# Performance work log

Measured on AMD Instinct MI355X. Metric: run time of the kernel, lower is better.

## Reference

```python
import jax, jax.numpy as jnp
import numpy as np

N = 50000      # num nodes
E = 800000     # num edges (before self loops)
B = 50         # num graphs in batch
F_IN = 15
C = 64         # hidden_channels
H = 4          # num_heads
NEG_SLOPE = 0.2  # PyG GATConv default


def setup_inputs() -> dict:
    key = jax.random.key(0)
    ks = jax.random.split(key, 32)
    s = 0.05
    inp = {
        "x": jax.random.normal(ks[0], (N, F_IN), dtype=jnp.float32),
        "edge_index": jax.random.randint(ks[1], (2, E), 0, N, dtype=jnp.int32),
        "batch": jnp.sort(jax.random.randint(ks[2], (N,), 0, B, dtype=jnp.int32)),
        "W1": jax.random.normal(ks[3], (F_IN, H * C)) * s,
        "aS1": jax.random.normal(ks[4], (H, C)) * s,
        "aD1": jax.random.normal(ks[5], (H, C)) * s,
        "b1": jnp.zeros((H * C,)),
        "W2": jax.random.normal(ks[6], (H * C, H * C)) * s,
        "aS2": jax.random.normal(ks[7], (H, C)) * s,
        "aD2": jax.random.normal(ks[8], (H, C)) * s,
        "b2": jnp.zeros((H * C,)),
        # GAT layer 3: 256 -> 64, 1 head
        "W3": jax.random.normal(ks[9], (H * C, C)) * s,
        "aS3": jax.random.normal(ks[10], (1, C)) * s,
        "aD3": jax.random.normal(ks[11], (1, C)) * s,
        "b3": jnp.zeros((C,)),
        # node attention MLP: 64 -> 32 -> 1
        "Wna1": jax.random.normal(ks[12], (C, 32)) * s,
        "bna1": jnp.zeros((32,)),
        "Wna2": jax.random.normal(ks[13], (32, 1)) * s,
        "bna2": jnp.zeros((1,)),
        # graph classifier: 128 -> 128 -> 64 -> 1
        "Wc1": jax.random.normal(ks[14], (2 * C, 128)) * s,
        "bc1": jnp.zeros((128,)),
        "Wc2": jax.random.normal(ks[15], (128, 64)) * s,
        "bc2": jnp.zeros((64,)),
        "Wc3": jax.random.normal(ks[16], (64, 1)) * s,
        "bc3": jnp.zeros((1,)),
    }
    return inp


def _gat_conv(x, src, dst, W, a_src, a_dst, b, heads, ch):
    """PyG-style GATConv (add_self_loops=True, negative_slope=0.2, eval mode)."""
    n = x.shape[0]
    h = (x @ W).reshape(n, heads, ch)               # [N, H, C]
    alpha_s = jnp.einsum('nhc,hc->nh', h, a_src)    # per-node src score
    alpha_d = jnp.einsum('nhc,hc->nh', h, a_dst)
    loops = jnp.arange(n, dtype=src.dtype)
    s = jnp.concatenate([src, loops])               # [E+N]
    d = jnp.concatenate([dst, loops])
    e = jax.nn.leaky_relu(alpha_s[s] + alpha_d[d], NEG_SLOPE)   # [E+N, H]
    # segment softmax over incoming edges of each dst node
    m = jax.ops.segment_max(e, d, num_segments=n)
    ex = jnp.exp(e - m[d])
    denom = jax.ops.segment_sum(ex, d, num_segments=n)
    alpha = ex / denom[d]                           # [E+N, H]
    msg = h[s] * alpha[:, :, None]                  # [E+N, H, C]
    out = jax.ops.segment_sum(msg, d, num_segments=n)  # [N, H, C]
    return out.reshape(n, heads * ch) + b


def reference(x, edge_index, batch, W1, aS1, aD1, b1, W2, aS2, aD2, b2,
              W3, aS3, aD3, b3, Wna1, bna1, Wna2, bna2,
              Wc1, bc1, Wc2, bc2, Wc3, bc3):
    src, dst = edge_index[0], edge_index[1]
    x1 = jax.nn.elu(_gat_conv(x, src, dst, W1, aS1, aD1, b1, H, C))
    x2 = jax.nn.elu(_gat_conv(x1, src, dst, W2, aS2, aD2, b2, H, C))
    x3 = jax.nn.elu(_gat_conv(x2, src, dst, W3, aS3, aD3, b3, 1, C))  # [N, 64]

    # node attention: MLP then softmax over ALL nodes (dim=0, as in source)
    na = jax.nn.relu(x3 @ Wna1 + bna1) @ Wna2 + bna2   # [N, 1]
    node_attention = jax.nn.softmax(na, axis=0)

    # graph pooling
    ones = jnp.ones((x3.shape[0],), dtype=x3.dtype)
    cnt = jax.ops.segment_sum(ones, batch, num_segments=B)         # [B]
    mean = jax.ops.segment_sum(x3, batch, num_segments=B) / jnp.maximum(cnt, 1.0)[:, None]
    mx = jax.ops.segment_max(x3, batch, num_segments=B)
    mx = jnp.where(cnt[:, None] > 0, mx, 0.0)
    g = jnp.concatenate([mean, mx], axis=1)                        # [B, 128]

    h1 = jax.nn.relu(g @ Wc1 + bc1)
    h2 = jax.nn.relu(h1 @ Wc2 + bc2)
    risk = jax.nn.sigmoid(h2 @ Wc3 + bc3)                          # [B, 1]
    return (risk, node_attention)
```

## Files before the change

### kernel.cpp

```cpp
#include <hip/hip_runtime.h>
#include <math.h>

#define NN 50000
#define EE 800000
#define ETOT (EE + NN)
#define BB 50
#define PC 16

typedef unsigned short u16;
typedef __attribute__((ext_vector_type(8))) short short8;
typedef __attribute__((ext_vector_type(4))) float floatx4;

__device__ __forceinline__ float b2f(u16 u) {
  return __int_as_float(((int)u) << 16);
}
__device__ __forceinline__ u16 f2b(float f) {
  unsigned u = __float_as_uint(f);
  unsigned r = (u + 0x7fffu + ((u >> 16) & 1u)) >> 16;
  return (u16)r;
}
__device__ __forceinline__ float readlane_f(float v, int l) {
  return __int_as_float(__builtin_amdgcn_readlane(__float_as_int(v), l));
}
__device__ __forceinline__ float blo(unsigned w) { return __uint_as_float(w << 16); }
__device__ __forceinline__ float bhi(unsigned w) { return __uint_as_float(w & 0xffff0000u); }

__global__ void count_kernel(const int* __restrict__ ei, int* __restrict__ cnt) {
  int e = blockIdx.x * blockDim.x + threadIdx.x;
  if (e >= ETOT) return;
  int d = (e < EE) ? ei[EE + e] : (e - EE);
  atomicAdd(&cnt[d], 1);
}

__global__ void scan1_kernel(const int* __restrict__ cnt, int* __restrict__ rowp,
                             int* __restrict__ part) {
  __shared__ int s[512];
  int t = threadIdx.x;
  int i = blockIdx.x * 512 + t;
  int v = (i < NN) ? cnt[i] : 0;
  s[t] = v;
  __syncthreads();
  for (int off = 1; off < 512; off <<= 1) {
    int add = (t >= off) ? s[t - off] : 0;
    __syncthreads();
    s[t] += add;
    __syncthreads();
  }
  if (i < NN) rowp[i] = s[t] - v;
  if (t == 511) part[blockIdx.x] = s[511];
}

__global__ void scan2_kernel(int* part, int* rowp) {
  int run = 0;
  for (int b = 0; b < 98; ++b) { int v = part[b]; part[b] = run; run += v; }
  rowp[NN] = run;
}

__global__ void scan3_kernel(int* __restrict__ rowp, const int* __restrict__ part) {
  int i = blockIdx.x * 512 + threadIdx.x;
  if (i < NN) rowp[i] += part[blockIdx.x];
}

__global__ void fill_kernel(const int* __restrict__ ei, const int* __restrict__ rowp,
                            int* __restrict__ cur, int* __restrict__ col) {
  int e = blockIdx.x * blockDim.x + threadIdx.x;
  if (e >= ETOT) return;
  int s, d;
  if (e < EE) { s = ei[e]; d = ei[EE + e]; } else { s = e - EE; d = s; }
  int p = atomicAdd(&cur[d], 1);
  col[rowp[d] + p] = s;
}

__global__ void prep_kernel(const float* __restrict__ x, const float* __restrict__ W1,
                            const float* __restrict__ W2, const float* __restrict__ W3,
                            u16* __restrict__ xb, u16* __restrict__ W1t,
                            u16* __restrict__ W2t, u16* __restrict__ W3t) {
  const int T0 = NN * 32, T1 = T0 + 8192, T2 = T1 + 65536, T3 = T2 + 16384;
  int i = blockIdx.x * 256 + threadIdx.x;
  if (i < T0) {
    int n = i >> 5, c = i & 31;
    xb[i] = (c < 15) ? f2b(x[n * 15 + c]) : (u16)0;
  } else if (i < T1) {
    int j = i - T0, n = j >> 5, k = j & 31;
    W1t[j] = (k < 15) ? f2b(W1[k * 256 + n]) : (u16)0;
  } else if (i < T2) {
    int j = i - T1, n = j >> 8, k = j & 255;
    W2t[j] = f2b(W2[k * 256 + n]);
  } else if (i < T3) {
    int j = i - T2, n = j >> 8, k = j & 255;
    W3t[j] = f2b(W3[k * 64 + n]);
  }
}

__global__ __launch_bounds__(256) void gemm_bf16_kernel(
    const u16* __restrict__ A, const u16* __restrict__ Bt, u16* __restrict__ C,
    int M, int K, int N) {
  __shared__ u16 Al[128][40];
  __shared__ u16 Bl[64][40];
  int R0 = blockIdx.x * 128, C0 = blockIdx.y * 64;
  int wid = threadIdx.x >> 6, lane = threadIdx.x & 63;
  int wr = (wid >> 1) * 64, wc = (wid & 1) * 32;
  int lrow = lane & 15, lk8 = (lane >> 4) * 8;
  floatx4 acc[4][2];
#pragma unroll
  for (int i = 0; i < 4; ++i)
#pragma unroll
    for (int j = 0; j < 2; ++j) acc[i][j] = (floatx4){0.f, 0.f, 0.f, 0.f};

  for (int k0 = 0; k0 < K; k0 += 32) {
#pragma unroll
    for (int c = threadIdx.x; c < 1024; c += 256) {
      int r = c >> 3, off = (c & 7) * 4;
      int gr = R0 + r;
      ushort4 va = make_ushort4(0, 0, 0, 0);
      if (gr < M) va = *(const ushort4*)&A[(size_t)gr * K + k0 + off];
      *(ushort4*)&Al[r][off] = va;
      if (c < 512)
        *(ushort4*)&Bl[r][off] = *(const ushort4*)&Bt[(size_t)(C0 + r) * K + k0 + off];
    }
    __syncthreads();
    short8 a[4], b[2];
#pragma unroll
    for (int i = 0; i < 4; ++i) a[i] = *(const short8*)&Al[wr + i * 16 + lrow][lk8];
#pragma unroll
    for (int j = 0; j < 2; ++j) b[j] = *(const short8*)&Bl[wc + j * 16 + lrow][lk8];
#pragma unroll
    for (int i = 0; i < 4; ++i)
#pragma unroll
      for (int j = 0; j < 2; ++j)
        acc[i][j] = __builtin_amdgcn_mfma_f32_16x16x32_bf16(a[i], b[j], acc[i][j], 0, 0, 0);
    __syncthreads();
  }
  int rq = (lane >> 4) * 4;
#pragma unroll
  for (int i = 0; i < 4; ++i)
#pragma unroll
    for (int j = 0; j < 2; ++j)
#pragma unroll
      for (int q = 0; q < 4; ++q) {
        int gr = R0 + wr + i * 16 + rq + q;
        if (gr < M) C[(size_t)gr * N + C0 + wc + j * 16 + lrow] = f2b(acc[i][j][q]);
      }
}

template <int H>
__global__ void score_kernel(const u16* __restrict__ h, const float* __restrict__ aS,
                             const float* __restrict__ aD, float* __restrict__ as_o,
                             float* __restrict__ ad_o) {
  const int CT = H * 64;
  int wid = threadIdx.x >> 6, lane = threadIdx.x & 63;
  int n = blockIdx.x * (blockDim.x >> 6) + wid;
  if (n >= NN) return;
  float ps[H], pd[H];
#pragma unroll
  for (int j = 0; j < H; ++j) {
    float hv = b2f(h[(size_t)n * CT + lane + 64 * j]);
    ps[j] = hv * aS[lane + 64 * j];
    pd[j] = hv * aD[lane + 64 * j];
  }
#pragma unroll
  for (int j = 0; j < H; ++j) {
    for (int o = 32; o; o >>= 1) {
      ps[j] += __shfl_xor(ps[j], o, 64);
      pd[j] += __shfl_xor(pd[j], o, 64);
    }
  }
  if (lane == 0) {
#pragma unroll
    for (int j = 0; j < H; ++j) {
      as_o[(size_t)n * H + j] = ps[j];
      ad_o[(size_t)n * H + j] = pd[j];
    }
  }
}

__global__ __launch_bounds__(256) void agg4_kernel(
    const u16* __restrict__ h, const float* __restrict__ as_i,
    const float* __restrict__ ad_i, const int* __restrict__ rowp,
    const int* __restrict__ col, const float* __restrict__ bias,
    u16* __restrict__ xo) {
  __shared__ float exs[4][64][4];
  int wid = threadIdx.x >> 6, lane = threadIdx.x & 63;
  int d = blockIdx.x * 4 + wid;
  int rp0 = rowp[d], deg = rowp[d + 1] - rp0;
  float4 add = *(const float4*)&ad_i[(size_t)d * 4];
  int hj = lane >> 4;
  int lq = lane << 2;
  float acc0 = 0.f, acc1 = 0.f, acc2 = 0.f, acc3 = 0.f;
  float den0 = 0.f, den1 = 0.f, den2 = 0.f, den3 = 0.f;

  for (int base = 0; base < deg; base += 64) {
    int i = base + lane;
    bool valid = i < deg;
    int s = valid ? col[rp0 + i] : 0;
    float4 asv = *(const float4*)&as_i[(size_t)s * 4];
    float e0 = asv.x + add.x, e1 = asv.y + add.y, e2 = asv.z + add.z, e3 = asv.w + add.w;
    e0 = (e0 > 0.f) ? e0 : 0.2f * e0;
    e1 = (e1 > 0.f) ? e1 : 0.2f * e1;
    e2 = (e2 > 0.f) ? e2 : 0.2f * e2;
    e3 = (e3 > 0.f) ? e3 : 0.2f * e3;
    float x0 = valid ? __expf(e0) : 0.f;
    float x1 = valid ? __expf(e1) : 0.f;
    float x2 = valid ? __expf(e2) : 0.f;
    float x3 = valid ? __expf(e3) : 0.f;
    den0 += x0; den1 += x1; den2 += x2; den3 += x3;
    *(float4*)&exs[wid][lane][0] = make_float4(x0, x1, x2, x3);
    __threadfence_block();
    int cnt = min(64, deg - base);
    int k4 = cnt & ~3;
    for (int k = 0; k < k4; k += 4) {
      int s0 = __builtin_amdgcn_readlane(s, k);
      int s1 = __builtin_amdgcn_readlane(s, k + 1);
      int s2 = __builtin_amdgcn_readlane(s, k + 2);
      int s3 = __builtin_amdgcn_readlane(s, k + 3);
      float q0 = exs[wid][k][hj];
      float q1 = exs[wid][k + 1][hj];
      float q2 = exs[wid][k + 2][hj];
      float q3 = exs[wid][k + 3][hj];
      uint2 w0 = *(const uint2*)&h[(size_t)s0 * 256 + lq];
      uint2 w1 = *(const uint2*)&h[(size_t)s1 * 256 + lq];
      uint2 w2 = *(const uint2*)&h[(size_t)s2 * 256 + lq];
      uint2 w3 = *(const uint2*)&h[(size_t)s3 * 256 + lq];
      acc0 += q0 * blo(w0.x); acc1 += q0 * bhi(w0.x);
      acc2 += q0 * blo(w0.y); acc3 += q0 * bhi(w0.y);
      acc0 += q1 * blo(w1.x); acc1 += q1 * bhi(w1.x);
      acc2 += q1 * blo(w1.y); acc3 += q1 * bhi(w1.y);
      acc0 += q2 * blo(w2.x); acc1 += q2 * bhi(w2.x);
      acc2 += q2 * blo(w2.y); acc3 += q2 * bhi(w2.y);
      acc0 += q3 * blo(w3.x); acc1 += q3 * bhi(w3.x);
      acc2 += q3 * blo(w3.y); acc3 += q3 * bhi(w3.y);
    }
    for (int k = k4; k < cnt; ++k) {
      int sk = __builtin_amdgcn_readlane(s, k);
      float qk = exs[wid][k][hj];
      uint2 wk = *(const uint2*)&h[(size_t)sk * 256 + lq];
      acc0 += qk * blo(wk.x); acc1 += qk * bhi(wk.x);
      acc2 += qk * blo(wk.y); acc3 += qk * bhi(wk.y);
    }
  }
#pragma unroll
  for (int o = 32; o; o >>= 1) {
    den0 += __shfl_xor(den0, o, 64);
    den1 += __shfl_xor(den1, o, 64);
    den2 += __shfl_xor(den2, o, 64);
    den3 += __shfl_xor(den3, o, 64);
  }
  float den = (hj == 0) ? den0 : (hj == 1) ? den1 : (hj == 2) ? den2 : den3;
  float inv = 1.f / den;
  float4 bv = *(const float4*)&bias[lq];
  float v0 = acc0 * inv + bv.x;
  float v1 = acc1 * inv + bv.y;
  float v2 = acc2 * inv + bv.z;
  float v3 = acc3 * inv + bv.w;
  v0 = (v0 > 0.f) ? v0 : expm1f(v0);
  v1 = (v1 > 0.f) ? v1 : expm1f(v1);
  v2 = (v2 > 0.f) ? v2 : expm1f(v2);
  v3 = (v3 > 0.f) ? v3 : expm1f(v3);
  ushort4 o4;
  o4.x = f2b(v0); o4.y = f2b(v1); o4.z = f2b(v2); o4.w = f2b(v3);
  ((ushort4*)xo)[(size_t)d * 64 + lane] = o4;
}

__global__ __launch_bounds__(256) void agg1_kernel(
    const u16* __restrict__ h, const float* __restrict__ as_i,
    const float* __restrict__ ad_i, const int* __restrict__ rowp,
    const int* __restrict__ col, const float* __restrict__ bias,
    float* __restrict__ xo) {
  int wid = threadIdx.x >> 6, lane = threadIdx.x & 63;
  int d = blockIdx.x * 4 + wid;
  int rp0 = rowp[d], deg = rowp[d + 1] - rp0;
  float add = ad_i[d];
  float acc = 0.f, den = 0.f;
  for (int base = 0; base < deg; base += 64) {
    int i = base + lane;
    bool valid = i < deg;
    int s = valid ? col[rp0 + i] : 0;
    float e = as_i[s] + add;
    e = (e > 0.f) ? e : 0.2f * e;
    float ex = valid ? __expf(e) : 0.f;
    den += ex;
    int cnt = min(64, deg - base);
    int k4 = cnt & ~3;
    for (int k = 0; k < k4; k += 4) {
      int s0 = __builtin_amdgcn_readlane(s, k);
      int s1 = __builtin_amdgcn_readlane(s, k + 1);
      int s2 = __builtin_amdgcn_readlane(s, k + 2);
      int s3 = __builtin_amdgcn_readlane(s, k + 3);
      float q0 = readlane_f(ex, k);
      float q1 = readlane_f(ex, k + 1);
      float q2 = readlane_f(ex, k + 2);
      float q3 = readlane_f(ex, k + 3);
      float h0 = b2f(h[(size_t)s0 * 64 + lane]);
      float h1 = b2f(h[(size_t)s1 * 64 + lane]);
      float h2 = b2f(h[(size_t)s2 * 64 + lane]);
      float h3 = b2f(h[(size_t)s3 * 64 + lane]);
      acc += q0 * h0 + q1 * h1 + q2 * h2 + q3 * h3;
    }
    for (int k = k4; k < cnt; ++k) {
      int sk = __builtin_amdgcn_readlane(s, k);
      float qk = readlane_f(ex, k);
      acc += qk * b2f(h[(size_t)sk * 64 + lane]);
    }
  }
#pragma unroll
  for (int o = 32; o; o >>= 1) den += __shfl_xor(den, o, 64);
  float v = acc / den + bias[lane];
  v = (v > 0.f) ? v : expm1f(v);
  xo[(size_t)d * 64 + lane] = v;
}

__global__ void na_kernel(const float* __restrict__ x3, const float* __restrict__ W1,
                          const float* __restrict__ b1, const float* __restrict__ W2,
                          const float* __restrict__ b2, float* __restrict__ na,
                          float* __restrict__ gsum) {
  __shared__ float Ws[64 * 32];
  __shared__ float W2s[32];
  __shared__ float sred[4];
  for (int i = threadIdx.x; i < 2048; i += blockDim.x) Ws[i] = W1[i];
  if (threadIdx.x < 32) W2s[threadIdx.x] = W2[threadIdx.x];
  __syncthreads();
  int n = blockIdx.x * blockDim.x + threadIdx.x;
  float ez = 0.f;
  if (n < NN) {
    float hid[32];
#pragma unroll
    for (int j = 0; j < 32; ++j) hid[j] = b1[j];
    for (int k = 0; k < 64; ++k) {
      float xv = x3[(size_t)n * 64 + k];
#pragma unroll
      for (int j = 0; j < 32; ++j) hid[j] += xv * Ws[k * 32 + j];
    }
    float z = b2[0];
#pragma unroll
    for (int j = 0; j < 32; ++j) z += fmaxf(hid[j], 0.f) * W2s[j];
    ez = __expf(z);
    na[n] = ez;
  }
  float acc = ez;
  for (int o = 32; o; o >>= 1) acc += __shfl_xor(acc, o, 64);
  int wid = threadIdx.x >> 6, lane = threadIdx.x & 63;
  if (lane == 0) sred[wid] = acc;
  __syncthreads();
  if (threadIdx.x == 0) atomicAdd(gsum, sred[0] + sred[1] + sred[2] + sred[3]);
}

__global__ void na_write_kernel(const float* __restrict__ na, const float* __restrict__ gsum,
                                float* __restrict__ out) {
  int n = blockIdx.x * blockDim.x + threadIdx.x;
  if (n >= NN) return;
  out[n] = na[n] / gsum[0];
}

__global__ void pool1_kernel(const float* __restrict__ x3, const int* __restrict__ batch,
                             float* __restrict__ ppsum, float* __restrict__ ppmax) {
  int b = blockIdx.x, c = blockIdx.y;
  int lane = threadIdx.x & 63, wid = threadIdx.x >> 6;
  int lo = 0, hi = NN;
  while (lo < hi) { int m = (lo + hi) >> 1; if (batch[m] < b) lo = m + 1; else hi = m; }
  int start = lo;
  lo = start; hi = NN;
  while (lo < hi) { int m = (lo + hi) >> 1; if (batch[m] < b + 1) lo = m + 1; else hi = m; }
  int end = lo;
  int len = end - start;
  int c0 = start + (int)((long)len * c / PC);
  int c1 = start + (int)((long)len * (c + 1) / PC);
  float acc = 0.f, mx = -INFINITY;
  for (int n = c0 + wid; n < c1; n += 4) {
    float v = x3[(size_t)n * 64 + lane];
    acc += v;
    mx = fmaxf(mx, v);
  }
  __shared__ float ssum[4][64], smax[4][64];
  ssum[wid][lane] = acc;
  smax[wid][lane] = mx;
  __syncthreads();
  if (wid == 0) {
    acc = ssum[0][lane] + ssum[1][lane] + ssum[2][lane] + ssum[3][lane];
    mx = fmaxf(fmaxf(smax[0][lane], smax[1][lane]), fmaxf(smax[2][lane], smax[3][lane]));
    size_t o = ((size_t)c * BB + b) * 64 + lane;
    ppsum[o] = acc;
    ppmax[o] = mx;
  }
}

__global__ void pool2_kernel(const float* __restrict__ ppsum, const float* __restrict__ ppmax,
                             const int* __restrict__ batch, float* __restrict__ psum,
                             float* __restrict__ pmax, float* __restrict__ pcnt) {
  int b = blockIdx.x, lane = threadIdx.x;
  float s = 0.f, m = -INFINITY;
#pragma unroll
  for (int c = 0; c < PC; ++c) {
    size_t o = ((size_t)c * BB + b) * 64 + lane;
    s += ppsum[o];
    m = fmaxf(m, ppmax[o]);
  }
  psum[b * 64 + lane] = s;
  pmax[b * 64 + lane] = m;
  if (lane == 0) {
    int lo = 0, hi = NN;
    while (lo < hi) { int mid = (lo + hi) >> 1; if (batch[mid] < b) lo = mid + 1; else hi = mid; }
    int start = lo;
    lo = start; hi = NN;
    while (lo < hi) { int mid = (lo + hi) >> 1; if (batch[mid] < b + 1) lo = mid + 1; else hi = mid; }
    pcnt[b] = (float)(lo - start);
  }
}

__global__ void cls_kernel(const float* __restrict__ psum, const float* __restrict__ pmax,
                           const float* __restrict__ pcnt, const float* __restrict__ Wc1,
                           const float* __restrict__ bc1, const float* __restrict__ Wc2,
                           const float* __restrict__ bc2, const float* __restrict__ Wc3,
                           const float* __restrict__ bc3, float* __restrict__ out) {
  __shared__ float g[128], h1[128], h2[64];
  int b = blockIdx.x, t = threadIdx.x;
  float cnt = pcnt[b];
  if (t < 64) {
    g[t] = (cnt > 0.f) ? psum[b * 64 + t] / fmaxf(cnt, 1.f) : 0.f;
    g[64 + t] = (cnt > 0.f) ? pmax[b * 64 + t] : 0.f;
  }
  __syncthreads();
  float v = bc1[t];
  for (int k = 0; k < 128; ++k) v += g[k] * Wc1[k * 128 + t];
  h1[t] = fmaxf(v, 0.f);
  __syncthreads();
  if (t < 64) {
    float v2 = bc2[t];
    for (int k = 0; k < 128; ++k) v2 += h1[k] * Wc2[k * 64 + t];
    h2[t] = fmaxf(v2, 0.f);
  }
  __syncthreads();
  if (t == 0) {
    float z = bc3[0];
    for (int k = 0; k < 64; ++k) z += h2[k] * Wc3[k];
    out[b] = 1.f / (1.f + expf(-z));
  }
}

extern "C" void kernel_launch(void* const* d_in, const int* in_sizes, int n_in,
                              void* d_out, int out_size, void* d_ws, size_t ws_size,
                              hipStream_t stream) {
  const float* x    = (const float*)d_in[0];
  const int*   ei   = (const int*)d_in[1];
  const int*   batch= (const int*)d_in[2];
  const float* W1 = (const float*)d_in[3];
  const float* aS1= (const float*)d_in[4];
  const float* aD1= (const float*)d_in[5];
  const float* b1 = (const float*)d_in[6];
  const float* W2 = (const float*)d_in[7];
  const float* aS2= (const float*)d_in[8];
  const float* aD2= (const float*)d_in[9];
  const float* b2 = (const float*)d_in[10];
  const float* W3 = (const float*)d_in[11];
  const float* aS3= (const float*)d_in[12];
  const float* aD3= (const float*)d_in[13];
  const float* b3 = (const float*)d_in[14];
  const float* Wna1=(const float*)d_in[15];
  const float* bna1=(const float*)d_in[16];
  const float* Wna2=(const float*)d_in[17];
  const float* bna2=(const float*)d_in[18];
  const float* Wc1=(const float*)d_in[19];
  const float* bc1=(const float*)d_in[20];
  const float* Wc2=(const float*)d_in[21];
  const float* bc2=(const float*)d_in[22];
  const float* Wc3=(const float*)d_in[23];
  const float* bc3=(const float*)d_in[24];
  float* out = (float*)d_out;

  char* w = (char*)d_ws;
  size_t off = 0;
  auto alloc = [&](size_t bytes) {
    void* p = w + off;
    off = (off + bytes + 255) & ~(size_t)255;
    return p;
  };
  u16* xb   = (u16*)alloc((size_t)NN * 32 * 2);
  u16* bufA = (u16*)alloc((size_t)NN * 256 * 2);
  u16* bufB = (u16*)alloc((size_t)NN * 256 * 2);
  u16* W1t  = (u16*)alloc((size_t)256 * 32 * 2);
  u16* W2t  = (u16*)alloc((size_t)256 * 256 * 2);
  u16* W3t  = (u16*)alloc((size_t)64 * 256 * 2);
  float* asb  = (float*)alloc((size_t)NN * 4 * 4);
  float* adb  = (float*)alloc((size_t)NN * 4 * 4);
  float* nab  = (float*)alloc((size_t)NN * 4);
  int* rowp = (int*)alloc((size_t)(NN + 1) * 4);
  int* cntb = (int*)alloc((size_t)NN * 4);
  int* curb = (int*)alloc((size_t)NN * 4);
  float* gsum = (float*)alloc(256);
  size_t zspan = (size_t)((char*)gsum + 256 - (char*)cntb);
  int* colb = (int*)alloc((size_t)ETOT * 4);
  int* part = (int*)alloc(98 * 4);
  float* psum = (float*)alloc((size_t)BB * 64 * 4);
  float* pmax = (float*)alloc((size_t)BB * 64 * 4);
  float* pcnt = (float*)alloc((size_t)BB * 4);
  float* ppsum = (float*)alloc((size_t)PC * BB * 64 * 4);
  float* ppmax = (float*)alloc((size_t)PC * BB * 64 * 4);
  float* x3 = (float*)bufB;
  (void)ws_size; (void)in_sizes; (void)n_in; (void)out_size;

  hipMemsetAsync(cntb, 0, zspan, stream);

  count_kernel<<<(ETOT + 255) / 256, 256, 0, stream>>>(ei, cntb);
  scan1_kernel<<<98, 512, 0, stream>>>(cntb, rowp, part);
  scan2_kernel<<<1, 1, 0, stream>>>(part, rowp);
  scan3_kernel<<<98, 512, 0, stream>>>(rowp, part);
  fill_kernel<<<(ETOT + 255) / 256, 256, 0, stream>>>(ei, rowp, curb, colb);

  const int PREP_TOT = NN * 32 + 8192 + 65536 + 16384;
  prep_kernel<<<(PREP_TOT + 255) / 256, 256, 0, stream>>>(x, W1, W2, W3, xb, W1t, W2t, W3t);

  const int GX = (NN + 127) / 128;
  gemm_bf16_kernel<<<dim3(GX, 4), 256, 0, stream>>>(xb, W1t, bufA, NN, 32, 256);
  score_kernel<4><<<12500, 256, 0, stream>>>(bufA, aS1, aD1, asb, adb);
  agg4_kernel<<<12500, 256, 0, stream>>>(bufA, asb, adb, rowp, colb, b1, bufB);
  gemm_bf16_kernel<<<dim3(GX, 4), 256, 0, stream>>>(bufB, W2t, bufA, NN, 256, 256);
  score_kernel<4><<<12500, 256, 0, stream>>>(bufA, aS2, aD2, asb, adb);
  agg4_kernel<<<12500, 256, 0, stream>>>(bufA, asb, adb, rowp, colb, b2, bufB);
  gemm_bf16_kernel<<<dim3(GX, 1), 256, 0, stream>>>(bufB, W3t, bufA, NN, 256, 64);
  score_kernel<1><<<12500, 256, 0, stream>>>(bufA, aS3, aD3, asb, adb);
  agg1_kernel<<<12500, 256, 0, stream>>>(bufA, asb, adb, rowp, colb, b3, x3);

  na_kernel<<<(NN + 255) / 256, 256, 0, stream>>>(x3, Wna1, bna1, Wna2, bna2, nab, gsum);
  na_write_kernel<<<(NN + 255) / 256, 256, 0, stream>>>(nab, gsum, out + BB);

  pool1_kernel<<<dim3(BB, PC), 256, 0, stream>>>(x3, batch, ppsum, ppmax);
  pool2_kernel<<<BB, 64, 0, stream>>>(ppsum, ppmax, batch, psum, pmax, pcnt);
  cls_kernel<<<BB, 128, 0, stream>>>(psum, pmax, pcnt, Wc1, bc1, Wc2, bc2, Wc3, bc3, out);
}
```

Baseline: 437.2 us.

## Fuse attention scores into GEMM epilogue, merge scans and pooling kernels

Computes per-node source/destination attention scores inside the bf16 GEMM epilogue using cross-lane shuffles, removing the three separate score kernels and their re-read of h. Rows are padded to a multiple of 128 so bounds checks in the GEMM go away, and K is tiled by 64 for the deeper layers. The three-kernel prefix scan becomes one single-block scan, pool2 and the classifier are merged, the agg1 gather loop is unrolled to 8, and the node-attention MLP loads x3 as float4. Costs are extra shared memory and shuffles in the GEMM, plus a single-block scan that runs serially over 49 elements per thread.

```diff
diff --git a/kernel.cpp b/kernel.cpp
--- a/kernel.cpp
+++ b/kernel.cpp
@@ -2,6 +2,7 @@
 #include <math.h>
 
 #define NN 50000
+#define NP 50176
 #define EE 800000
 #define ETOT (EE + NN)
 #define BB 50
@@ -32,33 +33,30 @@
   atomicAdd(&cnt[d], 1);
 }
 
-__global__ void scan1_kernel(const int* __restrict__ cnt, int* __restrict__ rowp,
-                             int* __restrict__ part) {
-  __shared__ int s[512];
+__global__ __launch_bounds__(1024) void scan_kernel(const int* __restrict__ cnt,
+                                                    int* __restrict__ rowp) {
+  __shared__ int part[1024];
   int t = threadIdx.x;
-  int i = blockIdx.x * 512 + t;
-  int v = (i < NN) ? cnt[i] : 0;
-  s[t] = v;
-  __syncthreads();
-  for (int off = 1; off < 512; off <<= 1) {
-    int add = (t >= off) ? s[t - off] : 0;
+  int base = t * 49;
+  int sum = 0;
+  for (int i = 0; i < 49; ++i) {
+    int idx = base + i;
+    if (idx < NN) sum += cnt[idx];
+  }
+  part[t] = sum;
+  __syncthreads();
+  for (int off = 1; off < 1024; off <<= 1) {
+    int add = (t >= off) ? part[t - off] : 0;
     __syncthreads();
-    s[t] += add;
+    part[t] += add;
     __syncthreads();
   }
-  if (i < NN) rowp[i] = s[t] - v;
-  if (t == 511) part[blockIdx.x] = s[511];
-}
-
-__global__ void scan2_kernel(int* part, int* rowp) {
-  int run = 0;
-  for (int b = 0; b < 98; ++b) { int v = part[b]; part[b] = run; run += v; }
-  rowp[NN] = run;
-}
-
-__global__ void scan3_kernel(int* __restrict__ rowp, const int* __restrict__ part) {
-  int i = blockIdx.x * 512 + threadIdx.x;
-  if (i < NN) rowp[i] += part[blockIdx.x];
+  int run = (t > 0) ? part[t - 1] : 0;
+  for (int i = 0; i < 49; ++i) {
+    int idx = base + i;
+    if (idx < NN) { rowp[idx] = run; run += cnt[idx]; }
+  }
+  if (t == 1023) rowp[NN] = part[1023];
 }
 
 __global__ void fill_kernel(const int* __restrict__ ei, const int* __restrict__ rowp,
@@ -75,11 +73,11 @@
                             const float* __restrict__ W2, const float* __restrict__ W3,
                             u16* __restrict__ xb, u16* __restrict__ W1t,
                             u16* __restrict__ W2t, u16* __restrict__ W3t) {
-  const int T0 = NN * 32, T1 = T0 + 8192, T2 = T1 + 65536, T3 = T2 + 16384;
+  const int T0 = NP * 32, T1 = T0 + 8192, T2 = T1 + 65536, T3 = T2 + 16384;
   int i = blockIdx.x * 256 + threadIdx.x;
   if (i < T0) {
     int n = i >> 5, c = i & 31;
-    xb[i] = (c < 15) ? f2b(x[n * 15 + c]) : (u16)0;
+    xb[i] = (n < NN && c < 15) ? f2b(x[n * 15 + c]) : (u16)0;
   } else if (i < T1) {
     int j = i - T0, n = j >> 5, k = j & 31;
     W1t[j] = (k < 15) ? f2b(W1[k * 256 + n]) : (u16)0;
@@ -92,46 +90,54 @@
   }
 }
 
+template <int BK>
 __global__ __launch_bounds__(256) void gemm_bf16_kernel(
     const u16* __restrict__ A, const u16* __restrict__ Bt, u16* __restrict__ C,
-    int M, int K, int N) {
-  __shared__ u16 Al[128][40];
-  __shared__ u16 Bl[64][40];
+    int K, int N, const float* __restrict__ aS, const float* __restrict__ aD,
+    float* __restrict__ as_o, float* __restrict__ ad_o, int Hh) {
+  __shared__ u16 Al[128][BK + 8];
+  __shared__ u16 Bl[64][BK + 8];
+  __shared__ float sS[4][64], sD[4][64];
   int R0 = blockIdx.x * 128, C0 = blockIdx.y * 64;
   int wid = threadIdx.x >> 6, lane = threadIdx.x & 63;
   int wr = (wid >> 1) * 64, wc = (wid & 1) * 32;
   int lrow = lane & 15, lk8 = (lane >> 4) * 8;
+  int rq = (lane >> 4) * 4;
+  const int Q4 = BK / 4;
+  const int nA = 128 * Q4, nB = 64 * Q4;
   floatx4 acc[4][2];
 #pragma unroll
   for (int i = 0; i < 4; ++i)
 #pragma unroll
     for (int j = 0; j < 2; ++j) acc[i][j] = (floatx4){0.f, 0.f, 0.f, 0.f};
 
-  for (int k0 = 0; k0 < K; k0 += 32) {
-#pragma unroll
-    for (int c = threadIdx.x; c < 1024; c += 256) {
-      int r = c >> 3, off = (c & 7) * 4;
-      int gr = R0 + r;
-      ushort4 va = make_ushort4(0, 0, 0, 0);
-      if (gr < M) va = *(const ushort4*)&A[(size_t)gr * K + k0 + off];
-      *(ushort4*)&Al[r][off] = va;
-      if (c < 512)
-        *(ushort4*)&Bl[r][off] = *(const ushort4*)&Bt[(size_t)(C0 + r) * K + k0 + off];
+  for (int k0 = 0; k0 < K; k0 += BK) {
+    for (int c = threadIdx.x; c < nA + nB; c += 256) {
+      if (c < nA) {
+        int r = c / Q4, o = (c % Q4) * 4;
+        *(ushort4*)&Al[r][o] = *(const ushort4*)&A[(size_t)(R0 + r) * K + k0 + o];
+      } else {
+        int c2 = c - nA;
+        int r = c2 / Q4, o = (c2 % Q4) * 4;
+        *(ushort4*)&Bl[r][o] = *(const ushort4*)&Bt[(size_t)(C0 + r) * K + k0 + o];
+      }
     }
     __syncthreads();
-    short8 a[4], b[2];
-#pragma unroll
-    for (int i = 0; i < 4; ++i) a[i] = *(const short8*)&Al[wr + i * 16 + lrow][lk8];
-#pragma unroll
-    for (int j = 0; j < 2; ++j) b[j] = *(const short8*)&Bl[wc + j * 16 + lrow][lk8];
-#pragma unroll
-    for (int i = 0; i < 4; ++i)
-#pragma unroll
-      for (int j = 0; j < 2; ++j)
-        acc[i][j] = __builtin_amdgcn_mfma_f32_16x16x32_bf16(a[i], b[j], acc[i][j], 0, 0, 0);
+#pragma unroll
+    for (int ks = 0; ks < BK / 32; ++ks) {
+      short8 a[4], b[2];
+#pragma unroll
+      for (int i = 0; i < 4; ++i) a[i] = *(const short8*)&Al[wr + i * 16 + lrow][ks * 32 + lk8];
+#pragma unroll
+      for (int j = 0; j < 2; ++j) b[j] = *(const short8*)&Bl[wc + j * 16 + lrow][ks * 32 + lk8];
+#pragma unroll
+      for (int i = 0; i < 4; ++i)
+#pragma unroll
+        for (int j = 0; j < 2; ++j)
+          acc[i][j] = __builtin_amdgcn_mfma_f32_16x16x32_bf16(a[i], b[j], acc[i][j], 0, 0, 0);
+    }
     __syncthreads();
   }
-  int rq = (lane >> 4) * 4;
 #pragma unroll
   for (int i = 0; i < 4; ++i)
 #pragma unroll
@@ -139,38 +145,34 @@
 #pragma unroll
       for (int q = 0; q < 4; ++q) {
         int gr = R0 + wr + i * 16 + rq + q;
-        if (gr < M) C[(size_t)gr * N + C0 + wc + j * 16 + lrow] = f2b(acc[i][j][q]);
+        C[(size_t)gr * N + C0 + wc + j * 16 + lrow] = f2b(acc[i][j][q]);
       }
-}
-
-template <int H>
-__global__ void score_kernel(const u16* __restrict__ h, const float* __restrict__ aS,
-                             const float* __restrict__ aD, float* __restrict__ as_o,
-                             float* __restrict__ ad_o) {
-  const int CT = H * 64;
-  int wid = threadIdx.x >> 6, lane = threadIdx.x & 63;
-  int n = blockIdx.x * (blockDim.x >> 6) + wid;
-  if (n >= NN) return;
-  float ps[H], pd[H];
-#pragma unroll
-  for (int j = 0; j < H; ++j) {
-    float hv = b2f(h[(size_t)n * CT + lane + 64 * j]);
-    ps[j] = hv * aS[lane + 64 * j];
-    pd[j] = hv * aD[lane + 64 * j];
-  }
-#pragma unroll
-  for (int j = 0; j < H; ++j) {
-    for (int o = 32; o; o >>= 1) {
-      ps[j] += __shfl_xor(ps[j], o, 64);
-      pd[j] += __shfl_xor(pd[j], o, 64);
-    }
-  }
-  if (lane == 0) {
-#pragma unroll
-    for (int j = 0; j < H; ++j) {
-      as_o[(size_t)n * H + j] = ps[j];
-      ad_o[(size_t)n * H + j] = pd[j];
-    }
+  int hb = blockIdx.y * 64;
+  float wS0 = aS[hb + wc + lrow], wS1 = aS[hb + wc + 16 + lrow];
+  float wD0 = aD[hb + wc + lrow], wD1 = aD[hb + wc + 16 + lrow];
+#pragma unroll
+  for (int i = 0; i < 4; ++i)
+#pragma unroll
+    for (int q = 0; q < 4; ++q) {
+      float vS = acc[i][0][q] * wS0 + acc[i][1][q] * wS1;
+      float vD = acc[i][0][q] * wD0 + acc[i][1][q] * wD1;
+#pragma unroll
+      for (int o = 8; o; o >>= 1) {
+        vS += __shfl_xor(vS, o, 64);
+        vD += __shfl_xor(vD, o, 64);
+      }
+      if (lrow == 0) {
+        int rl = i * 16 + rq + q;
+        sS[wid][rl] = vS;
+        sD[wid][rl] = vD;
+      }
+    }
+  __syncthreads();
+  if (threadIdx.x < 128) {
+    int p = threadIdx.x >> 6, r = threadIdx.x & 63;
+    int gr = R0 + p * 64 + r;
+    as_o[(size_t)gr * Hh + blockIdx.y] = sS[2 * p][r] + sS[2 * p + 1][r];
+    ad_o[(size_t)gr * Hh + blockIdx.y] = sD[2 * p][r] + sD[2 * p + 1][r];
   }
 }
 
@@ -280,23 +282,24 @@
     float ex = valid ? __expf(e) : 0.f;
     den += ex;
     int cnt = min(64, deg - base);
-    int k4 = cnt & ~3;
-    for (int k = 0; k < k4; k += 4) {
-      int s0 = __builtin_amdgcn_readlane(s, k);
-      int s1 = __builtin_amdgcn_readlane(s, k + 1);
-      int s2 = __builtin_amdgcn_readlane(s, k + 2);
-      int s3 = __builtin_amdgcn_readlane(s, k + 3);
-      float q0 = readlane_f(ex, k);
-      float q1 = readlane_f(ex, k + 1);
-      float q2 = readlane_f(ex, k + 2);
-      float q3 = readlane_f(ex, k + 3);
-      float h0 = b2f(h[(size_t)s0 * 64 + lane]);
-      float h1 = b2f(h[(size_t)s1 * 64 + lane]);
-      float h2 = b2f(h[(size_t)s2 * 64 + lane]);
-      float h3 = b2f(h[(size_t)s3 * 64 + lane]);
-      acc += q0 * h0 + q1 * h1 + q2 * h2 + q3 * h3;
-    }
-    for (int k = k4; k < cnt; ++k) {
+    int k8 = cnt & ~7;
+    for (int k = 0; k < k8; k += 8) {
+      int sA[8];
+      float qA[8], hv[8];
+#pragma unroll
+      for (int u = 0; u < 8; ++u) {
+        sA[u] = __builtin_amdgcn_readlane(s, k + u);
+        qA[u] = readlane_f(ex, k + u);
+      }
+#pragma unroll
+      for (int u = 0; u < 8; ++u) hv[u] = b2f(h[(size_t)sA[u] * 64 + lane]);
+      float p0 = qA[0] * hv[0] + qA[1] * hv[1];
+      float p1 = qA[2] * hv[2] + qA[3] * hv[3];
+      float p2 = qA[4] * hv[4] + qA[5] * hv[5];
+      float p3 = qA[6] * hv[6] + qA[7] * hv[7];
+      acc += (p0 + p1) + (p2 + p3);
+    }
+    for (int k = k8; k < cnt; ++k) {
       int sk = __builtin_amdgcn_readlane(s, k);
       float qk = readlane_f(ex, k);
       acc += qk * b2f(h[(size_t)sk * 64 + lane]);
@@ -325,10 +328,16 @@
     float hid[32];
 #pragma unroll
     for (int j = 0; j < 32; ++j) hid[j] = b1[j];
-    for (int k = 0; k < 64; ++k) {
-      float xv = x3[(size_t)n * 64 + k];
-#pragma unroll
-      for (int j = 0; j < 32; ++j) hid[j] += xv * Ws[k * 32 + j];
+    const float4* x4 = (const float4*)&x3[(size_t)n * 64];
+    for (int kk = 0; kk < 16; ++kk) {
+      float4 xv = x4[kk];
+#pragma unroll
+      for (int j = 0; j < 32; ++j) {
+        hid[j] += xv.x * Ws[(kk * 4 + 0) * 32 + j];
+        hid[j] += xv.y * Ws[(kk * 4 + 1) * 32 + j];
+        hid[j] += xv.z * Ws[(kk * 4 + 2) * 32 + j];
+        hid[j] += xv.w * Ws[(kk * 4 + 3) * 32 + j];
+      }
     }
     float z = b2[0];
 #pragma unroll
@@ -383,40 +392,35 @@
   }
 }
 
-__global__ void pool2_kernel(const float* __restrict__ ppsum, const float* __restrict__ ppmax,
-                             const int* __restrict__ batch, float* __restrict__ psum,
-                             float* __restrict__ pmax, float* __restrict__ pcnt) {
-  int b = blockIdx.x, lane = threadIdx.x;
-  float s = 0.f, m = -INFINITY;
-#pragma unroll
-  for (int c = 0; c < PC; ++c) {
-    size_t o = ((size_t)c * BB + b) * 64 + lane;
-    s += ppsum[o];
-    m = fmaxf(m, ppmax[o]);
-  }
-  psum[b * 64 + lane] = s;
-  pmax[b * 64 + lane] = m;
-  if (lane == 0) {
+__global__ void pool2cls_kernel(const float* __restrict__ ppsum, const float* __restrict__ ppmax,
+                                const int* __restrict__ batch, const float* __restrict__ Wc1,
+                                const float* __restrict__ bc1, const float* __restrict__ Wc2,
+                                const float* __restrict__ bc2, const float* __restrict__ Wc3,
+                                const float* __restrict__ bc3, float* __restrict__ out) {
+  __shared__ float g[128], h1[128], h2[64], scnt;
+  int b = blockIdx.x, t = threadIdx.x;
+  if (t == 0) {
     int lo = 0, hi = NN;
-    while (lo < hi) { int mid = (lo + hi) >> 1; if (batch[mid] < b) lo = mid + 1; else hi = mid; }
+    while (lo < hi) { int m = (lo + hi) >> 1; if (batch[m] < b) lo = m + 1; else hi = m; }
     int start = lo;
     lo = start; hi = NN;
-    while (lo < hi) { int mid = (lo + hi) >> 1; if (batch[mid] < b + 1) lo = mid + 1; else hi = mid; }
-    pcnt[b] = (float)(lo - start);
-  }
-}
-
-__global__ void cls_kernel(const float* __restrict__ psum, const float* __restrict__ pmax,
-                           const float* __restrict__ pcnt, const float* __restrict__ Wc1,
-                           const float* __restrict__ bc1, const float* __restrict__ Wc2,
-                           const float* __restrict__ bc2, const float* __restrict__ Wc3,
-                           const float* __restrict__ bc3, float* __restrict__ out) {
-  __shared__ float g[128], h1[128], h2[64];
-  int b = blockIdx.x, t = threadIdx.x;
-  float cnt = pcnt[b];
+    while (lo < hi) { int m = (lo + hi) >> 1; if (batch[m] < b + 1) lo = m + 1; else hi = m; }
+    scnt = (float)(lo - start);
+  }
+  float s = 0.f, m = -INFINITY;
   if (t < 64) {
-    g[t] = (cnt > 0.f) ? psum[b * 64 + t] / fmaxf(cnt, 1.f) : 0.f;
-    g[64 + t] = (cnt > 0.f) ? pmax[b * 64 + t] : 0.f;
+#pragma unroll
+    for (int c = 0; c < PC; ++c) {
+      size_t o = ((size_t)c * BB + b) * 64 + t;
+      s += ppsum[o];
+      m = fmaxf(m, ppmax[o]);
+    }
+  }
+  __syncthreads();
+  float cnt = scnt;
+  if (t < 64) {
+    g[t] = (cnt > 0.f) ? s / fmaxf(cnt, 1.f) : 0.f;
+    g[64 + t] = (cnt > 0.f) ? m : 0.f;
   }
   __syncthreads();
   float v = bc1[t];
@@ -473,14 +477,14 @@
     off = (off + bytes + 255) & ~(size_t)255;
     return p;
   };
-  u16* xb   = (u16*)alloc((size_t)NN * 32 * 2);
-  u16* bufA = (u16*)alloc((size_t)NN * 256 * 2);
-  u16* bufB = (u16*)alloc((size_t)NN * 256 * 2);
+  u16* xb   = (u16*)alloc((size_t)NP * 32 * 2);
+  u16* bufA = (u16*)alloc((size_t)NP * 256 * 2);
+  u16* bufB = (u16*)alloc((size_t)NP * 256 * 2);
   u16* W1t  = (u16*)alloc((size_t)256 * 32 * 2);
   u16* W2t  = (u16*)alloc((size_t)256 * 256 * 2);
   u16* W3t  = (u16*)alloc((size_t)64 * 256 * 2);
-  float* asb  = (float*)alloc((size_t)NN * 4 * 4);
-  float* adb  = (float*)alloc((size_t)NN * 4 * 4);
+  float* asb  = (float*)alloc((size_t)NP * 4 * 4);
+  float* adb  = (float*)alloc((size_t)NP * 4 * 4);
   float* nab  = (float*)alloc((size_t)NN * 4);
   int* rowp = (int*)alloc((size_t)(NN + 1) * 4);
   int* cntb = (int*)alloc((size_t)NN * 4);
@@ -488,10 +492,6 @@
   float* gsum = (float*)alloc(256);
   size_t zspan = (size_t)((char*)gsum + 256 - (char*)cntb);
   int* colb = (int*)alloc((size_t)ETOT * 4);
-  int* part = (int*)alloc(98 * 4);
-  float* psum = (float*)alloc((size_t)BB * 64 * 4);
-  float* pmax = (float*)alloc((size_t)BB * 64 * 4);
-  float* pcnt = (float*)alloc((size_t)BB * 4);
   float* ppsum = (float*)alloc((size_t)PC * BB * 64 * 4);
   float* ppmax = (float*)alloc((size_t)PC * BB * 64 * 4);
   float* x3 = (float*)bufB;
@@ -500,29 +500,27 @@
   hipMemsetAsync(cntb, 0, zspan, stream);
 
   count_kernel<<<(ETOT + 255) / 256, 256, 0, stream>>>(ei, cntb);
-  scan1_kernel<<<98, 512, 0, stream>>>(cntb, rowp, part);
-  scan2_kernel<<<1, 1, 0, stream>>>(part, rowp);
-  scan3_kernel<<<98, 512, 0, stream>>>(rowp, part);
+  scan_kernel<<<1, 1024, 0, stream>>>(cntb, rowp);
   fill_kernel<<<(ETOT + 255) / 256, 256, 0, stream>>>(ei, rowp, curb, colb);
 
-  const int PREP_TOT = NN * 32 + 8192 + 65536 + 16384;
+  const int PREP_TOT = NP * 32 + 8192 + 65536 + 16384;
   prep_kernel<<<(PREP_TOT + 255) / 256, 256, 0, stream>>>(x, W1, W2, W3, xb, W1t, W2t, W3t);
 
-  const int GX = (NN + 127) / 128;
-  gemm_bf16_kernel<<<dim3(GX, 4), 256, 0, stream>>>(xb, W1t, bufA, NN, 32, 256);
-  score_kernel<4><<<12500, 256, 0, stream>>>(bufA, aS1, aD1, asb, adb);
+  const int GX = NP / 128;
+  gemm_bf16_kernel<32><<<dim3(GX, 4), 256, 0, stream>>>(xb, W1t, bufA, 32, 256,
+                                                        aS1, aD1, asb, adb, 4);
   agg4_kernel<<<12500, 256, 0, stream>>>(bufA, asb, adb, rowp, colb, b1, bufB);
-  gemm_bf16_kernel<<<dim3(GX, 4), 256, 0, stream>>>(bufB, W2t, bufA, NN, 256, 256);
-  score_kernel<4><<<12500, 256, 0, stream>>>(bufA, aS2, aD2, asb, adb);
+  gemm_bf16_kernel<64><<<dim3(GX, 4), 256, 0, stream>>>(bufB, W2t, bufA, 256, 256,
+                                                        aS2, aD2, asb, adb, 4);
   agg4_kernel<<<12500, 256, 0, stream>>>(bufA, asb, adb, rowp, colb, b2, bufB);
-  gemm_bf16_kernel<<<dim3(GX, 1), 256, 0, stream>>>(bufB, W3t, bufA, NN, 256, 64);
-  score_kernel<1><<<12500, 256, 0, stream>>>(bufA, aS3, aD3, asb, adb);
+  gemm_bf16_kernel<64><<<dim3(GX, 1), 256, 0, stream>>>(bufB, W3t, bufA, 256, 64,
+                                                        aS3, aD3, asb, adb, 1);
   agg1_kernel<<<12500, 256, 0, stream>>>(bufA, asb, adb, rowp, colb, b3, x3);
 
   na_kernel<<<(NN + 255) / 256, 256, 0, stream>>>(x3, Wna1, bna1, Wna2, bna2, nab, gsum);
   na_write_kernel<<<(NN + 255) / 256, 256, 0, stream>>>(nab, gsum, out + BB);
 
   pool1_kernel<<<dim3(BB, PC), 256, 0, stream>>>(x3, batch, ppsum, ppmax);
-  pool2_kernel<<<BB, 64, 0, stream>>>(ppsum, ppmax, batch, psum, pmax, pcnt);
-  cls_kernel<<<BB, 128, 0, stream>>>(psum, pmax, pcnt, Wc1, bc1, Wc2, bc2, Wc3, bc3, out);
-}
+  pool2cls_kernel<<<BB, 128, 0, stream>>>(ppsum, ppmax, batch, Wc1, bc1, Wc2, bc2,
+                                          Wc3, bc3, out);
+}
```

Result: slower. 475.7 us (+8.8%).
